# Optimization experiments

Hardware: AMD Instinct MI355X
Metric: run time of the kernel (lower is better)

Reference implementation:

```python
import jax, jax.numpy as jnp
import numpy as np

N_NODES = 100000
N_EDGES = 1600000
F_IN, HIDDEN, N_CLASS = 64, 48, 40


def setup_inputs() -> dict:
    key = jax.random.key(0)
    ks = jax.random.split(key, 9)
    def glorot(k, fi, fo):
        s = (6.0 / (fi + fo)) ** 0.5
        return jax.random.uniform(k, (fi, fo), jnp.float32, -s, s)
    return {
        "x": jax.random.normal(ks[0], (N_NODES, F_IN), jnp.float32),
        "edge_index": jax.random.randint(ks[1], (2, N_EDGES), 0, N_NODES, jnp.int64),
        "edge_weight": jax.random.uniform(ks[2], (N_EDGES,), jnp.float32),
        "W1": glorot(ks[3], F_IN, HIDDEN),   # ARMAConv init_weight (K=1)
        "V1": glorot(ks[4], F_IN, HIDDEN),   # ARMAConv root_weight
        "b1": jnp.zeros((HIDDEN,), jnp.float32),
        "W2": glorot(ks[5], HIDDEN, N_CLASS),
        "V2": glorot(ks[6], HIDDEN, N_CLASS),
        "b2": jnp.zeros((N_CLASS,), jnp.float32),
    }


def _arma_conv(x, W, V, b, src, dst, norm, num_nodes):
    # out = ReLU( A_norm @ (x @ W) + x @ V + b )   (num_stacks=1, num_layers=1)
    h = x @ W                                   # [N, F_out]
    msg = h[src] * norm[:, None]                # gather + scale  [E, F_out]
    agg = jax.ops.segment_sum(msg, dst, num_segments=num_nodes)  # scatter-add
    return jax.nn.relu(agg + x @ V + b)


def reference(x, edge_index, edge_weight, W1, V1, b1, W2, V2, b2):
    num_nodes = x.shape[0]
    src, dst = edge_index[0], edge_index[1]
    # gcn_norm, add_self_loops=False: D^{-1/2} A D^{-1/2}
    deg = jax.ops.segment_sum(edge_weight, dst, num_segments=num_nodes)
    dinv = jnp.where(deg > 0, jax.lax.rsqrt(jnp.where(deg > 0, deg, 1.0)), 0.0)
    norm = dinv[src] * edge_weight * dinv[dst]
    # eval mode: input dropout is identity
    h = _arma_conv(x, W1, V1, b1, src, dst, norm, num_nodes)
    h = _arma_conv(h, W2, V2, b2, src, dst, norm, num_nodes)
    return jax.nn.log_softmax(h, axis=-1)
```

## Files before the change

### kernel.cpp

```cpp
#include <hip/hip_runtime.h>
#include <math.h>


constexpr int F_IN = 64;
constexpr int HIDDEN = 48;
constexpr int N_CLASS = 40;
constexpr int CHUNK = 2048;
constexpr int EPT = CHUNK / 256;
constexpr int BIN_SHIFT = 7;
constexpr int BIN_CAP = 2560;
constexpr int MAXBINS = 1024;

typedef __attribute__((ext_vector_type(8))) short bf16x8;
typedef __attribute__((ext_vector_type(4))) float f32x4;

__device__ __forceinline__ short bfr(float f) {
    unsigned u = __float_as_uint(f);
    return (short)((u + 0x7fffu + ((u >> 16) & 1u)) >> 16);
}
__device__ __forceinline__ unsigned pack_bf2(float a, float b) {
    unsigned ua = __float_as_uint(a), ub = __float_as_uint(b);
    ua = (ua + 0x7fffu + ((ua >> 16) & 1u)) >> 16;
    ub = (ub + 0x7fffu + ((ub >> 16) & 1u)) >> 16;
    return ua | (ub << 16);
}
__device__ __forceinline__ float2 unpack_bf2(unsigned u) {
    return make_float2(__uint_as_float(u << 16), __uint_as_float(u & 0xffff0000u));
}
__device__ __forceinline__ bf16x8 cvt8(float4 f0, float4 f1) {
    bf16x8 r;
    r[0] = bfr(f0.x); r[1] = bfr(f0.y); r[2] = bfr(f0.z); r[3] = bfr(f0.w);
    r[4] = bfr(f1.x); r[5] = bfr(f1.y); r[6] = bfr(f1.z); r[7] = bfr(f1.w);
    return r;
}

__global__ void init_cursor(int* __restrict__ binCursor) {
    binCursor[threadIdx.x] = (int)threadIdx.x * BIN_CAP;
}

__global__ __launch_bounds__(256) void gemm1_kernel(
    const float* __restrict__ X, const float* __restrict__ W,
    const float* __restrict__ V, const float* __restrict__ b,
    unsigned* __restrict__ XWp, unsigned* __restrict__ AGGp, int N) {
    __shared__ char smem[36864];
    short* sWT = (short*)smem;
    float* ep = (float*)(smem + 12288);
    int tid = threadIdx.x;
    for (int i = tid; i < 96 * 64; i += 256) {
        int c = i >> 6, k = i & 63;
        float v = (c < 48) ? W[k * 48 + c] : V[k * 48 + (c - 48)];
        sWT[i] = bfr(v);
    }
    __syncthreads();

    int lane = tid & 63, wv = tid >> 6;
    int m = lane & 15, quad = lane >> 4;
    int nb0 = (int)blockIdx.x * 64;
    int n = nb0 + wv * 16 + m;

    bf16x8 a0, a1;
    if (n < N) {
        const float4* xr = (const float4*)(X + (size_t)n * 64 + quad * 8);
        a0 = cvt8(xr[0], xr[1]);
        const float4* xr2 = (const float4*)(X + (size_t)n * 64 + 32 + quad * 8);
        a1 = cvt8(xr2[0], xr2[1]);
    } else {
        for (int j = 0; j < 8; ++j) { a0[j] = 0; a1[j] = 0; }
    }

    f32x4 acc[6];
#pragma unroll
    for (int ct = 0; ct < 6; ++ct) acc[ct] = (f32x4){0.f, 0.f, 0.f, 0.f};
#pragma unroll
    for (int ct = 0; ct < 6; ++ct) {
        bf16x8 b0 = *(const bf16x8*)(sWT + (ct * 16 + m) * 64 + quad * 8);
        bf16x8 b1 = *(const bf16x8*)(sWT + (ct * 16 + m) * 64 + 32 + quad * 8);
        acc[ct] = __builtin_amdgcn_mfma_f32_16x16x32_bf16(a0, b0, acc[ct], 0, 0, 0);
        acc[ct] = __builtin_amdgcn_mfma_f32_16x16x32_bf16(a1, b1, acc[ct], 0, 0, 0);
    }
#pragma unroll
    for (int ct = 0; ct < 6; ++ct)
#pragma unroll
        for (int r = 0; r < 4; ++r)
            ep[(wv * 16 + quad * 4 + r) * 96 + ct * 16 + m] = acc[ct][r];
    __syncthreads();
    for (int i = tid; i < 64 * 24; i += 256) {
        int r = i / 24, c2 = i - r * 24;
        int node = nb0 + r;
        if (node >= N) continue;
        float w0 = ep[r * 96 + 2 * c2], w1 = ep[r * 96 + 2 * c2 + 1];
        XWp[node * 24 + c2] = pack_bf2(w0, w1);
        float v0 = ep[r * 96 + 48 + 2 * c2], v1 = ep[r * 96 + 48 + 2 * c2 + 1];
        float2 bb = ((const float2*)b)[c2];
        AGGp[node * 24 + c2] = pack_bf2(v0 + bb.x, v1 + bb.y);
    }
}

__global__ __launch_bounds__(256) void binscatter(
    const int* __restrict__ src, const int* __restrict__ dst,
    const float* __restrict__ w, int* __restrict__ binCursor,
    int2* __restrict__ binned, int E, int NB) {
    __shared__ int hist[MAXBINS];
    int tid = threadIdx.x;
    for (int j = tid; j < NB; j += 256) hist[j] = 0;
    __syncthreads();
    long long e0 = (long long)blockIdx.x * CHUNK;
    int M = (int)min((long long)CHUNK, (long long)E - e0);
    int dv[EPT], sv[EPT], wv[EPT];
#pragma unroll
    for (int q = 0; q < EPT; ++q) {
        int i = tid + q * 256;
        if (i < M) {
            dv[q] = dst[e0 + i];
            sv[q] = src[e0 + i];
            wv[q] = __float_as_int(w[e0 + i]);
            atomicAdd(&hist[dv[q] >> BIN_SHIFT], 1);
        }
    }
    __syncthreads();
    for (int j = tid; j < NB; j += 256) {
        int h = hist[j];
        hist[j] = h ? atomicAdd(&binCursor[j], h) : 0;
    }
    __syncthreads();
#pragma unroll
    for (int q = 0; q < EPT; ++q) {
        int i = tid + q * 256;
        if (i < M) {
            int d = dv[q];
            int p = atomicAdd(&hist[d >> BIN_SHIFT], 1);
            binned[p] = make_int2(((d & (BIN_CAP - 1) & 127) << 17) | sv[q], wv[q]);
        }
    }
}

__global__ __launch_bounds__(256) void build_csr(const int2* __restrict__ binned,
                                                 const int* __restrict__ binCursor,
                                                 int* __restrict__ rowBeg,
                                                 int* __restrict__ rowEnd,
                                                 float* __restrict__ dinv,
                                                 unsigned* __restrict__ csr,
                                                 unsigned* __restrict__ XW1p, int N) {
    __shared__ int cntL[128];
    __shared__ float degL[128];
    __shared__ int scanL[128];
    int b = blockIdx.x, tid = threadIdx.x;
    int e0 = b * BIN_CAP;
    int M = min(binCursor[b] - e0, BIN_CAP);
    if (tid < 128) { cntL[tid] = 0; degL[tid] = 0.f; }
    __syncthreads();
    for (int i = tid; i < M; i += 256) {
        int2 p = binned[e0 + i];
        int dl = ((unsigned)p.x) >> 17;
        atomicAdd(&cntL[dl], 1);
        atomicAdd(&degL[dl], __int_as_float(p.y));
    }
    __syncthreads();
    int v = 0;
    if (tid < 128) { v = cntL[tid]; scanL[tid] = v; }
    __syncthreads();
#pragma unroll
    for (int o = 1; o < 128; o <<= 1) {
        int u = (tid < 128 && tid >= o) ? scanL[tid - o] : 0;
        __syncthreads();
        if (tid < 128) scanL[tid] += u;
        __syncthreads();
    }
    if (tid < 128) {
        int excl = scanL[tid] - v;
        int node = (b << BIN_SHIFT) + tid;
        float dg = degL[tid];
        float dvv = dg > 0.f ? rsqrtf(dg) : 0.f;
        if (node < N) {
            rowBeg[node] = e0 + excl;
            rowEnd[node] = e0 + excl + v;
            dinv[node] = dvv;
        }
        cntL[tid] = e0 + excl;
        degL[tid] = dvv;
    }
    __syncthreads();
    for (int i = tid; i < M; i += 256) {
        int2 p = binned[e0 + i];
        int dl = ((unsigned)p.x) >> 17;
        int pos = atomicAdd(&cntL[dl], 1);
        float wn = __int_as_float(p.y) * degL[dl];
        unsigned uw = __float_as_uint(wn);
        uw = (uw + 0x7fffu + ((uw >> 16) & 1u)) >> 16;
        csr[pos] = ((unsigned)(p.x & 0x1FFFF) << 15) | uw;
    }
    int nb0 = b << BIN_SHIFT;
    for (int i = tid; i < 128 * 24; i += 256) {
        int nl = i / 24, c = i - nl * 24;
        int nn = nb0 + nl;
        if (nn >= N) break;
        float dvn = degL[nl];
        float2 u = unpack_bf2(XW1p[nn * 24 + c]);
        XW1p[nn * 24 + c] = pack_bf2(u.x * dvn, u.y * dvn);
    }
}

template <int W>
__device__ __forceinline__ void edge4(const unsigned* __restrict__ XWp, uint4 p4,
                                      int c, float4& s) {
    uint2 u0 = *(const uint2*)(XWp + (p4.x >> 15) * W + c);
    uint2 u1 = *(const uint2*)(XWp + (p4.y >> 15) * W + c);
    uint2 u2 = *(const uint2*)(XWp + (p4.z >> 15) * W + c);
    uint2 u3 = *(const uint2*)(XWp + (p4.w >> 15) * W + c);
    float n0 = __uint_as_float((p4.x & 0x7FFFu) << 16);
    float n1 = __uint_as_float((p4.y & 0x7FFFu) << 16);
    float n2 = __uint_as_float((p4.z & 0x7FFFu) << 16);
    float n3 = __uint_as_float((p4.w & 0x7FFFu) << 16);
    float2 a0 = unpack_bf2(u0.x), b0 = unpack_bf2(u0.y);
    float2 a1 = unpack_bf2(u1.x), b1 = unpack_bf2(u1.y);
    float2 a2 = unpack_bf2(u2.x), b2 = unpack_bf2(u2.y);
    float2 a3 = unpack_bf2(u3.x), b3 = unpack_bf2(u3.y);
    s.x = fmaf(a0.x, n0, s.x); s.y = fmaf(a0.y, n0, s.y);
    s.z = fmaf(b0.x, n0, s.z); s.w = fmaf(b0.y, n0, s.w);
    s.x = fmaf(a1.x, n1, s.x); s.y = fmaf(a1.y, n1, s.y);
    s.z = fmaf(b1.x, n1, s.z); s.w = fmaf(b1.y, n1, s.w);
    s.x = fmaf(a2.x, n2, s.x); s.y = fmaf(a2.y, n2, s.y);
    s.z = fmaf(b2.x, n2, s.z); s.w = fmaf(b2.y, n2, s.w);
    s.x = fmaf(a3.x, n3, s.x); s.y = fmaf(a3.y, n3, s.y);
    s.z = fmaf(b3.x, n3, s.z); s.w = fmaf(b3.y, n3, s.w);
}

template <int W>
__device__ __forceinline__ float4 row_accum2(const unsigned* __restrict__ XWp,
                                             const unsigned* __restrict__ csr,
                                             int j, int end, int c, float4 s) {
    while (j < end && (j & 3)) {
        unsigned p = csr[j++];
        uint2 u = *(const uint2*)(XWp + (p >> 15) * W + c);
        float nr = __uint_as_float((p & 0x7FFFu) << 16);
        float2 x0 = unpack_bf2(u.x), x1 = unpack_bf2(u.y);
        s.x = fmaf(x0.x, nr, s.x); s.y = fmaf(x0.y, nr, s.y);
        s.z = fmaf(x1.x, nr, s.z); s.w = fmaf(x1.y, nr, s.w);
    }
    int nch = (end - j) >> 2;
    if (nch > 0) {
        uint4 p4 = *(const uint4*)(csr + j);
        for (int k = 1; k < nch; ++k) {
            uint4 p4n = *(const uint4*)(csr + j + (k << 2));
            edge4<W>(XWp, p4, c, s);
            p4 = p4n;
        }
        edge4<W>(XWp, p4, c, s);
        j += nch << 2;
    }
    for (; j < end; ++j) {
        unsigned p = csr[j];
        uint2 u = *(const uint2*)(XWp + (p >> 15) * W + c);
        float nr = __uint_as_float((p & 0x7FFFu) << 16);
        float2 x0 = unpack_bf2(u.x), x1 = unpack_bf2(u.y);
        s.x = fmaf(x0.x, nr, s.x); s.y = fmaf(x0.y, nr, s.y);
        s.z = fmaf(x1.x, nr, s.z); s.w = fmaf(x1.y, nr, s.w);
    }
    return s;
}

__global__ __launch_bounds__(384) void pull_agg(const unsigned* __restrict__ XWp,
                                                const unsigned* __restrict__ csr,
                                                const int* __restrict__ rowBeg,
                                                const int* __restrict__ rowEnd,
                                                const unsigned* __restrict__ AGG1p,
                                                unsigned* __restrict__ H1p, int N) {
    int t = blockIdx.x * blockDim.x + threadIdx.x;
    int n = t / 12, c1 = t - n * 12;
    if (n >= N) return;
    int c = 2 * c1;
    uint2 a = *(const uint2*)(AGG1p + n * 24 + c);
    float2 f0 = unpack_bf2(a.x), f1 = unpack_bf2(a.y);
    float4 s = make_float4(f0.x, f0.y, f1.x, f1.y);
    s = row_accum2<24>(XWp, csr, rowBeg[n], rowEnd[n], c, s);
    uint2 o;
    o.x = pack_bf2(fmaxf(s.x, 0.f), fmaxf(s.y, 0.f));
    o.y = pack_bf2(fmaxf(s.z, 0.f), fmaxf(s.w, 0.f));
    *(uint2*)(H1p + n * 24 + c) = o;
}

__global__ __launch_bounds__(256) void gemm2_kernel(
    const short* __restrict__ H1, const float* __restrict__ W,
    const float* __restrict__ V, const float* __restrict__ b,
    const float* __restrict__ dinv, unsigned* __restrict__ XWp,
    unsigned* __restrict__ AGGp, int N) {
    __shared__ char smem[30720];
    short* sWT = (short*)smem;
    float* ep = (float*)(smem + 10240);
    int tid = threadIdx.x;
    for (int i = tid; i < 80 * 64; i += 256) {
        int c = i >> 6, k = i & 63;
        float v = 0.f;
        if (k < 48) v = (c < 40) ? W[k * 40 + c] : V[k * 40 + (c - 40)];
        sWT[i] = bfr(v);
    }
    __syncthreads();

    int lane = tid & 63, wv = tid >> 6;
    int m = lane & 15, quad = lane >> 4;
    int nb0 = (int)blockIdx.x * 64;
    int n = nb0 + wv * 16 + m;

    bf16x8 a0, a1;
    if (n < N) {
        a0 = *(const bf16x8*)(H1 + (size_t)n * 48 + quad * 8);
        if (quad < 2) {
            a1 = *(const bf16x8*)(H1 + (size_t)n * 48 + 32 + quad * 8);
        } else {
            for (int j = 0; j < 8; ++j) a1[j] = 0;
        }
    } else {
        for (int j = 0; j < 8; ++j) { a0[j] = 0; a1[j] = 0; }
    }

    f32x4 acc[5];
#pragma unroll
    for (int ct = 0; ct < 5; ++ct) acc[ct] = (f32x4){0.f, 0.f, 0.f, 0.f};
#pragma unroll
    for (int ct = 0; ct < 5; ++ct) {
        bf16x8 b0 = *(const bf16x8*)(sWT + (ct * 16 + m) * 64 + quad * 8);
        bf16x8 b1 = *(const bf16x8*)(sWT + (ct * 16 + m) * 64 + 32 + quad * 8);
        acc[ct] = __builtin_amdgcn_mfma_f32_16x16x32_bf16(a0, b0, acc[ct], 0, 0, 0);
        acc[ct] = __builtin_amdgcn_mfma_f32_16x16x32_bf16(a1, b1, acc[ct], 0, 0, 0);
    }
#pragma unroll
    for (int ct = 0; ct < 5; ++ct)
#pragma unroll
        for (int r = 0; r < 4; ++r)
            ep[(wv * 16 + quad * 4 + r) * 80 + ct * 16 + m] = acc[ct][r];
    __syncthreads();
    for (int i = tid; i < 64 * 20; i += 256) {
        int r = i / 20, c2 = i - r * 20;
        int node = nb0 + r;
        if (node >= N) continue;
        float dv = dinv[node];
        float w0 = ep[r * 80 + 2 * c2], w1 = ep[r * 80 + 2 * c2 + 1];
        XWp[node * 20 + c2] = pack_bf2(w0 * dv, w1 * dv);
        float v0 = ep[r * 80 + 40 + 2 * c2], v1 = ep[r * 80 + 40 + 2 * c2 + 1];
        float2 bb = ((const float2*)b)[c2];
        AGGp[node * 20 + c2] = pack_bf2(v0 + bb.x, v1 + bb.y);
    }
}

__global__ __launch_bounds__(320) void pull_ls(const unsigned* __restrict__ XWp,
                                               const unsigned* __restrict__ csr,
                                               const int* __restrict__ rowBeg,
                                               const int* __restrict__ rowEnd,
                                               const unsigned* __restrict__ AGG2p,
                                               float* __restrict__ out, int N) {
    __shared__ float4 sbuf[32 * 10];
    __shared__ float sl[32];
    int tid = threadIdx.x;
    int nl = tid / 10, c1 = tid - nl * 10;
    int n = blockIdx.x * 32 + nl;
    int c = 2 * c1;
    float4 s = make_float4(0.f, 0.f, 0.f, 0.f);
    if (n < N) {
        uint2 a = *(const uint2*)(AGG2p + n * 20 + c);
        float2 f0 = unpack_bf2(a.x), f1 = unpack_bf2(a.y);
        s = make_float4(f0.x, f0.y, f1.x, f1.y);
        s = row_accum2<20>(XWp, csr, rowBeg[n], rowEnd[n], c, s);
    }
    sbuf[nl * 10 + c1] = s;
    __syncthreads();
    if (tid < 32) {
        float m = 0.f;
        for (int k = 0; k < 10; ++k) {
            float4 v = sbuf[tid * 10 + k];
            m = fmaxf(m, fmaxf(fmaxf(v.x, v.y), fmaxf(v.z, v.w)));
        }
        float sum = 0.f;
        for (int k = 0; k < 10; ++k) {
            float4 v = sbuf[tid * 10 + k];
            sum += expf(fmaxf(v.x, 0.f) - m) + expf(fmaxf(v.y, 0.f) - m) +
                   expf(fmaxf(v.z, 0.f) - m) + expf(fmaxf(v.w, 0.f) - m);
        }
        sl[tid] = m + logf(sum);
    }
    __syncthreads();
    if (n < N) {
        float l = sl[nl];
        ((float4*)out)[n * 10 + c1] =
            make_float4(fmaxf(s.x, 0.f) - l, fmaxf(s.y, 0.f) - l,
                        fmaxf(s.z, 0.f) - l, fmaxf(s.w, 0.f) - l);
    }
}

extern "C" void kernel_launch(void* const* d_in, const int* in_sizes, int n_in,
                              void* d_out, int out_size, void* d_ws, size_t ws_size,
                              hipStream_t stream) {
    const float* x  = (const float*)d_in[0];
    const int*   ei = (const int*)d_in[1];
    const float* ew = (const float*)d_in[2];
    const float* W1 = (const float*)d_in[3];
    const float* V1 = (const float*)d_in[4];
    const float* b1 = (const float*)d_in[5];
    const float* W2 = (const float*)d_in[6];
    const float* V2 = (const float*)d_in[7];
    const float* b2 = (const float*)d_in[8];
    float* out = (float*)d_out;

    const int N = in_sizes[0] / F_IN;
    const int E = in_sizes[2];
    const int* src = ei;
    const int* dst = ei + E;

    char* ws = (char*)d_ws;
    size_t off = 0;
    auto carve = [&](size_t bytes) {
        void* p = ws + off;
        off = (off + bytes + 255) & ~size_t(255);
        return p;
    };
    auto cdiv = [](long long a, long long b) { return (int)((a + b - 1) / b); };
    const int nBins = cdiv(N, 1 << BIN_SHIFT);

    int*      binCursor = (int*)carve(MAXBINS * 4);
    int*      rowBeg    = (int*)carve((size_t)N * 4);
    int*      rowEnd    = (int*)carve((size_t)N * 4);
    float*    dinv      = (float*)carve((size_t)N * 4);
    int2*     binned    = (int2*)carve((size_t)nBins * BIN_CAP * 8);
    unsigned* csr       = (unsigned*)carve((size_t)nBins * BIN_CAP * 4);
    unsigned* xW1p      = (unsigned*)carve((size_t)N * 24 * 4);
    unsigned* agg1p     = (unsigned*)carve((size_t)N * 24 * 4);
    unsigned* h1p       = (unsigned*)carve((size_t)N * 24 * 4);
    unsigned* xW2p      = (unsigned*)carve((size_t)N * 20 * 4);
    unsigned* agg2p     = (unsigned*)carve((size_t)N * 20 * 4);

    const int B = 256;
    const int nSc = cdiv(E, CHUNK);
    const int nGemmBlocks = cdiv(N, 64);

    init_cursor<<<1, MAXBINS, 0, stream>>>(binCursor);
    binscatter<<<nSc, B, 0, stream>>>(src, dst, ew, binCursor, binned, E, nBins);
    gemm1_kernel<<<nGemmBlocks, B, 0, stream>>>(x, W1, V1, b1, xW1p, agg1p, N);
    build_csr<<<nBins, 256, 0, stream>>>(binned, binCursor, rowBeg, rowEnd,
                                         dinv, csr, xW1p, N);

    pull_agg<<<cdiv((long long)N * 12, 384), 384, 0, stream>>>(xW1p, csr, rowBeg,
                                                               rowEnd, agg1p, h1p, N);

    gemm2_kernel<<<nGemmBlocks, B, 0, stream>>>((const short*)h1p, W2, V2, b2,
                                                dinv, xW2p, agg2p, N);

    pull_ls<<<cdiv(N, 32), 320, 0, stream>>>(xW2p, csr, rowBeg, rowEnd,
                                             agg2p, out, N);
}
```

Baseline: 277.5 us.

## Build CSR via global atomics and three-pass scan instead of bin scatter

Replaces the two-level binning CSR construction with direct global atomic degree counting, a three-kernel prefix scan over 4-padded row counts, and a per-edge atomic cursor scatter into the CSR array. The dinv scaling of XW1 moves into gemm1's epilogue, which removes the read-modify-write pass in build_csr. This trades the locality of shared-memory binning for many global atomics with random addresses and more kernel launches. Rows are padded to multiples of 4, presumably so that vectorised uint4 edge loads stay aligned.

Result: slower. 444.4 us (+60.2%).

```diff
diff --git a/kernel.cpp b/kernel.cpp
--- a/kernel.cpp
+++ b/kernel.cpp
@@ -5,11 +5,6 @@
 constexpr int F_IN = 64;
 constexpr int HIDDEN = 48;
 constexpr int N_CLASS = 40;
-constexpr int CHUNK = 2048;
-constexpr int EPT = CHUNK / 256;
-constexpr int BIN_SHIFT = 7;
-constexpr int BIN_CAP = 2560;
-constexpr int MAXBINS = 1024;
 
 typedef __attribute__((ext_vector_type(8))) short bf16x8;
 typedef __attribute__((ext_vector_type(4))) float f32x4;
@@ -34,13 +29,109 @@
     return r;
 }
 
-__global__ void init_cursor(int* __restrict__ binCursor) {
-    binCursor[threadIdx.x] = (int)threadIdx.x * BIN_CAP;
+__global__ __launch_bounds__(256) void zero_cd(int* __restrict__ cnt,
+                                               float* __restrict__ deg, int NP) {
+    int i = blockIdx.x * 256 + threadIdx.x;
+    if (i < NP) { cnt[i] = 0; deg[i] = 0.f; }
+}
+
+__global__ __launch_bounds__(256) void deg_count(const int* __restrict__ dst,
+                                                 const float* __restrict__ w,
+                                                 int* __restrict__ cnt,
+                                                 float* __restrict__ deg, int E) {
+    int i = blockIdx.x * 256 + threadIdx.x;
+    if (i < E) {
+        int d = dst[i];
+        atomicAdd(&cnt[d], 1);
+        atomicAdd(&deg[d], w[i]);
+    }
+}
+
+__global__ __launch_bounds__(256) void scan1(const int4* __restrict__ cnt4,
+                                             int* __restrict__ tPre,
+                                             int* __restrict__ bSum) {
+    __shared__ int scanL[256];
+    int b = blockIdx.x, tid = threadIdx.x;
+    int4 c = cnt4[b * 256 + tid];
+    int s = ((c.x + 3) & ~3) + ((c.y + 3) & ~3) + ((c.z + 3) & ~3) + ((c.w + 3) & ~3);
+    scanL[tid] = s;
+    __syncthreads();
+#pragma unroll
+    for (int o = 1; o < 256; o <<= 1) {
+        int u = (tid >= o) ? scanL[tid - o] : 0;
+        __syncthreads();
+        scanL[tid] += u;
+        __syncthreads();
+    }
+    tPre[b * 256 + tid] = scanL[tid] - s;
+    if (tid == 255) bSum[b] = scanL[255];
+}
+
+__global__ __launch_bounds__(128) void scan2(const int* __restrict__ bSum,
+                                             int* __restrict__ bOff, int NB) {
+    __shared__ int scanL[128];
+    int tid = threadIdx.x;
+    int v = (tid < NB) ? bSum[tid] : 0;
+    scanL[tid] = v;
+    __syncthreads();
+#pragma unroll
+    for (int o = 1; o < 128; o <<= 1) {
+        int u = (tid >= o) ? scanL[tid - o] : 0;
+        __syncthreads();
+        scanL[tid] += u;
+        __syncthreads();
+    }
+    if (tid < NB) bOff[tid] = scanL[tid] - v;
+}
+
+__global__ __launch_bounds__(256) void scan3(const int4* __restrict__ cnt4,
+                                             const float* __restrict__ deg,
+                                             const int* __restrict__ tPre,
+                                             const int* __restrict__ bOff,
+                                             int* __restrict__ rowBeg,
+                                             int* __restrict__ rowEnd,
+                                             int* __restrict__ cursor,
+                                             float* __restrict__ dinv, int N) {
+    int b = blockIdx.x, tid = threadIdx.x;
+    int4 c = cnt4[b * 256 + tid];
+    int base = bOff[b] + tPre[b * 256 + tid];
+    int n0 = (b * 256 + tid) * 4;
+    int cc[4] = {c.x, c.y, c.z, c.w};
+#pragma unroll
+    for (int k = 0; k < 4; ++k) {
+        int n = n0 + k;
+        if (n < N) {
+            rowBeg[n] = base;
+            rowEnd[n] = base + cc[k];
+            cursor[n] = base;
+            float dg = deg[n];
+            dinv[n] = dg > 0.f ? rsqrtf(dg) : 0.f;
+        }
+        base += (cc[k] + 3) & ~3;
+    }
+}
+
+__global__ __launch_bounds__(256) void scatter_csr(const int* __restrict__ src,
+                                                   const int* __restrict__ dst,
+                                                   const float* __restrict__ w,
+                                                   const float* __restrict__ dinv,
+                                                   int* __restrict__ cursor,
+                                                   unsigned* __restrict__ csr, int E) {
+    int i = blockIdx.x * 256 + threadIdx.x;
+    if (i < E) {
+        int d = dst[i];
+        int pos = atomicAdd(&cursor[d], 1);
+        float wn = w[i] * dinv[d];
+        unsigned uw = __float_as_uint(wn);
+        uw = (uw + 0x7fffu + ((uw >> 16) & 1u)) >> 16;
+        csr[pos] = ((unsigned)(src[i] & 0x1FFFF) << 15) | uw;
+    }
 }
 
 __global__ __launch_bounds__(256) void gemm1_kernel(
     const float* __restrict__ X, const float* __restrict__ W,
     const float* __restrict__ V, const float* __restrict__ b,
+    const float* __restrict__ dinv,
     unsigned* __restrict__ XWp, unsigned* __restrict__ AGGp, int N) {
     __shared__ char smem[36864];
     short* sWT = (short*)smem;
@@ -88,115 +179,12 @@
         int r = i / 24, c2 = i - r * 24;
         int node = nb0 + r;
         if (node >= N) continue;
+        float dv = dinv[node];
         float w0 = ep[r * 96 + 2 * c2], w1 = ep[r * 96 + 2 * c2 + 1];
-        XWp[node * 24 + c2] = pack_bf2(w0, w1);
+        XWp[node * 24 + c2] = pack_bf2(w0 * dv, w1 * dv);
         float v0 = ep[r * 96 + 48 + 2 * c2], v1 = ep[r * 96 + 48 + 2 * c2 + 1];
         float2 bb = ((const float2*)b)[c2];
         AGGp[node * 24 + c2] = pack_bf2(v0 + bb.x, v1 + bb.y);
-    }
-}
-
-__global__ __launch_bounds__(256) void binscatter(
-    const int* __restrict__ src, const int* __restrict__ dst,
-    const float* __restrict__ w, int* __restrict__ binCursor,
-    int2* __restrict__ binned, int E, int NB) {
-    __shared__ int hist[MAXBINS];
-    int tid = threadIdx.x;
-    for (int j = tid; j < NB; j += 256) hist[j] = 0;
-    __syncthreads();
-    long long e0 = (long long)blockIdx.x * CHUNK;
-    int M = (int)min((long long)CHUNK, (long long)E - e0);
-    int dv[EPT], sv[EPT], wv[EPT];
-#pragma unroll
-    for (int q = 0; q < EPT; ++q) {
-        int i = tid + q * 256;
-        if (i < M) {
-            dv[q] = dst[e0 + i];
-            sv[q] = src[e0 + i];
-            wv[q] = __float_as_int(w[e0 + i]);
-            atomicAdd(&hist[dv[q] >> BIN_SHIFT], 1);
-        }
-    }
-    __syncthreads();
-    for (int j = tid; j < NB; j += 256) {
-        int h = hist[j];
-        hist[j] = h ? atomicAdd(&binCursor[j], h) : 0;
-    }
-    __syncthreads();
-#pragma unroll
-    for (int q = 0; q < EPT; ++q) {
-        int i = tid + q * 256;
-        if (i < M) {
-            int d = dv[q];
-            int p = atomicAdd(&hist[d >> BIN_SHIFT], 1);
-            binned[p] = make_int2(((d & (BIN_CAP - 1) & 127) << 17) | sv[q], wv[q]);
-        }
-    }
-}
-
-__global__ __launch_bounds__(256) void build_csr(const int2* __restrict__ binned,
-                                                 const int* __restrict__ binCursor,
-                                                 int* __restrict__ rowBeg,
-                                                 int* __restrict__ rowEnd,
-                                                 float* __restrict__ dinv,
-                                                 unsigned* __restrict__ csr,
-                                                 unsigned* __restrict__ XW1p, int N) {
-    __shared__ int cntL[128];
-    __shared__ float degL[128];
-    __shared__ int scanL[128];
-    int b = blockIdx.x, tid = threadIdx.x;
-    int e0 = b * BIN_CAP;
-    int M = min(binCursor[b] - e0, BIN_CAP);
-    if (tid < 128) { cntL[tid] = 0; degL[tid] = 0.f; }
-    __syncthreads();
-    for (int i = tid; i < M; i += 256) {
-        int2 p = binned[e0 + i];
-        int dl = ((unsigned)p.x) >> 17;
-        atomicAdd(&cntL[dl], 1);
-        atomicAdd(&degL[dl], __int_as_float(p.y));
-    }
-    __syncthreads();
-    int v = 0;
-    if (tid < 128) { v = cntL[tid]; scanL[tid] = v; }
-    __syncthreads();
-#pragma unroll
-    for (int o = 1; o < 128; o <<= 1) {
-        int u = (tid < 128 && tid >= o) ? scanL[tid - o] : 0;
-        __syncthreads();
-        if (tid < 128) scanL[tid] += u;
-        __syncthreads();
-    }
-    if (tid < 128) {
-        int excl = scanL[tid] - v;
-        int node = (b << BIN_SHIFT) + tid;
-        float dg = degL[tid];
-        float dvv = dg > 0.f ? rsqrtf(dg) : 0.f;
-        if (node < N) {
-            rowBeg[node] = e0 + excl;
-            rowEnd[node] = e0 + excl + v;
-            dinv[node] = dvv;
-        }
-        cntL[tid] = e0 + excl;
-        degL[tid] = dvv;
-    }
-    __syncthreads();
-    for (int i = tid; i < M; i += 256) {
-        int2 p = binned[e0 + i];
-        int dl = ((unsigned)p.x) >> 17;
-        int pos = atomicAdd(&cntL[dl], 1);
-        float wn = __int_as_float(p.y) * degL[dl];
-        unsigned uw = __float_as_uint(wn);
-        uw = (uw + 0x7fffu + ((uw >> 16) & 1u)) >> 16;
-        csr[pos] = ((unsigned)(p.x & 0x1FFFF) << 15) | uw;
-    }
-    int nb0 = b << BIN_SHIFT;
-    for (int i = tid; i < 128 * 24; i += 256) {
-        int nl = i / 24, c = i - nl * 24;
-        int nn = nb0 + nl;
-        if (nn >= N) break;
-        float dvn = degL[nl];
-        float2 u = unpack_bf2(XW1p[nn * 24 + c]);
-        XW1p[nn * 24 + c] = pack_bf2(u.x * dvn, u.y * dvn);
     }
 }
 
@@ -405,6 +393,10 @@
     const int* src = ei;
     const int* dst = ei + E;
 
+    auto cdiv = [](long long a, long long b) { return (int)((a + b - 1) / b); };
+    const int NB1 = cdiv(N, 1024);
+    const int NPAD = NB1 * 1024;
+
     char* ws = (char*)d_ws;
     size_t off = 0;
     auto carve = [&](size_t bytes) {
@@ -412,30 +404,33 @@
         off = (off + bytes + 255) & ~size_t(255);
         return p;
     };
-    auto cdiv = [](long long a, long long b) { return (int)((a + b - 1) / b); };
-    const int nBins = cdiv(N, 1 << BIN_SHIFT);
-
-    int*      binCursor = (int*)carve(MAXBINS * 4);
-    int*      rowBeg    = (int*)carve((size_t)N * 4);
-    int*      rowEnd    = (int*)carve((size_t)N * 4);
-    float*    dinv      = (float*)carve((size_t)N * 4);
-    int2*     binned    = (int2*)carve((size_t)nBins * BIN_CAP * 8);
-    unsigned* csr       = (unsigned*)carve((size_t)nBins * BIN_CAP * 4);
-    unsigned* xW1p      = (unsigned*)carve((size_t)N * 24 * 4);
-    unsigned* agg1p     = (unsigned*)carve((size_t)N * 24 * 4);
-    unsigned* h1p       = (unsigned*)carve((size_t)N * 24 * 4);
-    unsigned* xW2p      = (unsigned*)carve((size_t)N * 20 * 4);
-    unsigned* agg2p     = (unsigned*)carve((size_t)N * 20 * 4);
+    int*      cnt    = (int*)carve((size_t)NPAD * 4);
+    float*    deg    = (float*)carve((size_t)NPAD * 4);
+    int*      tPre   = (int*)carve((size_t)NB1 * 256 * 4);
+    int*      bSum   = (int*)carve(128 * 4);
+    int*      bOff   = (int*)carve(128 * 4);
+    int*      rowBeg = (int*)carve((size_t)N * 4);
+    int*      rowEnd = (int*)carve((size_t)N * 4);
+    int*      cursor = (int*)carve((size_t)N * 4);
+    float*    dinv   = (float*)carve((size_t)N * 4);
+    unsigned* csr    = (unsigned*)carve(((size_t)E + 3 * N + 64) * 4);
+    unsigned* xW1p   = (unsigned*)carve((size_t)N * 24 * 4);
+    unsigned* agg1p  = (unsigned*)carve((size_t)N * 24 * 4);
+    unsigned* h1p    = (unsigned*)carve((size_t)N * 24 * 4);
+    unsigned* xW2p   = (unsigned*)carve((size_t)N * 20 * 4);
+    unsigned* agg2p  = (unsigned*)carve((size_t)N * 20 * 4);
 
     const int B = 256;
-    const int nSc = cdiv(E, CHUNK);
     const int nGemmBlocks = cdiv(N, 64);
 
-    init_cursor<<<1, MAXBINS, 0, stream>>>(binCursor);
-    binscatter<<<nSc, B, 0, stream>>>(src, dst, ew, binCursor, binned, E, nBins);
-    gemm1_kernel<<<nGemmBlocks, B, 0, stream>>>(x, W1, V1, b1, xW1p, agg1p, N);
-    build_csr<<<nBins, 256, 0, stream>>>(binned, binCursor, rowBeg, rowEnd,
-                                         dinv, csr, xW1p, N);
+    zero_cd<<<cdiv(NPAD, B), B, 0, stream>>>(cnt, deg, NPAD);
+    deg_count<<<cdiv(E, B), B, 0, stream>>>(dst, ew, cnt, deg, E);
+    scan1<<<NB1, 256, 0, stream>>>((const int4*)cnt, tPre, bSum);
+    scan2<<<1, 128, 0, stream>>>(bSum, bOff, NB1);
+    scan3<<<NB1, 256, 0, stream>>>((const int4*)cnt, deg, tPre, bOff,
+                                   rowBeg, rowEnd, cursor, dinv, N);
+    gemm1_kernel<<<nGemmBlocks, B, 0, stream>>>(x, W1, V1, b1, dinv, xW1p, agg1p, N);
+    scatter_csr<<<cdiv(E, B), B, 0, stream>>>(src, dst, ew, dinv, cursor, csr, E);
 
     pull_agg<<<cdiv((long long)N * 12, 384), 384, 0, stream>>>(xW1p, csr, rowBeg,
                                                                rowEnd, agg1p, h1p, N);
```
